# Performance work log

Measured on AMD Instinct MI355X. Metric: run time of the kernel, lower is better.

Reference implementation:

```python
import jax, jax.numpy as jnp
import numpy as np

B, S, D = 2, 2048, 2048
NH, NKV = 16, 4
HD = D // NH          # 128
Q_DIM = NH * HD       # 2048
KV_DIM = NKV * HD     # 512
N_REP = NH // NKV     # 4


def setup_inputs() -> dict:
    key = jax.random.key(0)
    k1, k2, k3, k4 = jax.random.split(key, 4)
    x = jax.random.normal(k1, (B, S, D), dtype=jnp.float32)
    freqs_cis = jax.random.normal(k2, (S, HD), dtype=jnp.float32)
    Wqkv = jax.random.normal(k3, (Q_DIM + 2 * KV_DIM, D), dtype=jnp.float32) * (D ** -0.5)
    Wo = jax.random.normal(k4, (D, Q_DIM), dtype=jnp.float32) * (Q_DIM ** -0.5)
    return {"x": x, "freqs_cis": freqs_cis, "Wqkv": Wqkv, "Wo": Wo}


def _apply_rope(xq, xk, freqs_cis):
    # xq: [B,S,NH,HD], xk: [B,S,NKV,HD], freqs_cis: [S,HD] viewed as [S,1,HD//2,2]
    f = freqs_cis.reshape(S, 1, HD // 2, 2)
    f0, f1 = f[..., 0], f[..., 1]  # broadcast over batch & heads

    def rot(t):
        shp = t.shape
        tp = t.reshape(*shp[:-1], HD // 2, 2)
        t0, t1 = tp[..., 0], tp[..., 1]
        # row1 = <x, (f0,f1)>;  row0 = <x, (f1,-f0)>  (matches torch flip+negate)
        row1 = t0 * f0 + t1 * f1
        row0 = t0 * f1 - t1 * f0
        return jnp.stack([row0, row1], axis=-1).reshape(shp)

    return rot(xq), rot(xk)


def reference(x, freqs_cis, Wqkv, Wo):
    # Fused QKV projection (exact path: all RLA sketch dims = 0)
    xqkv = jnp.einsum('bsd,od->bso', x, Wqkv)
    xq = xqkv[..., :Q_DIM].reshape(B, S, NH, HD)
    xk = xqkv[..., Q_DIM:Q_DIM + KV_DIM].reshape(B, S, NKV, HD)
    xv = xqkv[..., Q_DIM + KV_DIM:].reshape(B, S, NKV, HD)

    xq, xk = _apply_rope(xq, xk, freqs_cis)

    # [B,H,S,HD]
    xq = xq.transpose(0, 2, 1, 3)
    xk = xk.transpose(0, 2, 1, 3)
    xv = xv.transpose(0, 2, 1, 3)

    # GQA: repeat kv heads n_rep times
    xk = jnp.repeat(xk, N_REP, axis=1)
    xv = jnp.repeat(xv, N_REP, axis=1)

    scale = 1.0 / jnp.sqrt(jnp.asarray(HD, dtype=xq.dtype))
    scores = jnp.einsum('bhqd,bhkd->bhqk', xq, xk) * scale
    causal = jnp.tril(jnp.ones((S, S), dtype=bool))
    scores = jnp.where(causal, scores, jnp.finfo(scores.dtype).min)
    probs = jax.nn.softmax(scores, axis=-1)
    out = jnp.einsum('bhqk,bhkd->bhqd', probs, xv)  # [B,H,S,HD]

    out = out.transpose(0, 2, 1, 3).reshape(B, S, Q_DIM)
    return jnp.einsum('bsq,dq->bsd', out, Wo)
```

## Files before the change

### kernel.cpp

```cpp
#include <hip/hip_runtime.h>
#include <hip/hip_bf16.h>
#include <cstdint>
#include <cstddef>

#define B_ 2
#define S_ 2048
#define NH_ 16
#define NKV_ 4
#define HD_ 128
#define QDIM_ 2048
#define KVDIM_ 512
#define QKV_ 3072

typedef __attribute__((ext_vector_type(8))) short short8;
typedef __attribute__((ext_vector_type(4))) float float4v;

__device__ __forceinline__ float bf2f(short u) {
  union { unsigned int i; float f; } v;
  v.i = ((unsigned int)(unsigned short)u) << 16;
  return v.f;
}
__device__ __forceinline__ short f2bf(float f) {
  union { float f; unsigned int i; } v; v.f = f;
  unsigned int x = v.i;
  x += 0x7fffu + ((x >> 16) & 1u);
  return (short)(x >> 16);
}

__device__ __forceinline__ void async_copy16(void* lds, const void* g) {
  __builtin_amdgcn_global_load_lds(
      (const __attribute__((address_space(1))) void*)g,
      (__attribute__((address_space(3))) void*)lds, 16, 0, 0);
}

__global__ void f32_to_bf16(const float* __restrict__ src, short* __restrict__ dst,
                            int n8) {
  int id = blockIdx.x * 256 + threadIdx.x;
  if (id >= n8) return;
  const float* f = src + (size_t)id * 8;
  float4v a = *(const float4v*)(f);
  float4v b = *(const float4v*)(f + 4);
  short8 r;
#pragma unroll
  for (int e = 0; e < 4; ++e) { r[e] = f2bf(a[e]); r[4 + e] = f2bf(b[e]); }
  *(short8*)(dst + (size_t)id * 8) = r;
}

template <int N, int K, bool CF32>
__global__ __launch_bounds__(256)
void gemm_nt_bf16(const short* __restrict__ A, const short* __restrict__ Bm,
                  void* __restrict__ Cp) {
  __shared__ __align__(16) short sA[128 * 32];
  __shared__ __align__(16) short sB[128 * 32];
  const int tid = threadIdx.x;
  const int m0 = blockIdx.y * 128, n0 = blockIdx.x * 128;
  const int wave = tid >> 6, lane = tid & 63;
  const int wm = (wave & 1) << 6, wn = (wave >> 1) << 6;
  const int lm = lane & 15, kg = lane >> 4;

  float4v acc[4][4];
#pragma unroll
  for (int i = 0; i < 4; ++i)
#pragma unroll
    for (int j = 0; j < 4; ++j)
      acc[i][j] = (float4v){0.f, 0.f, 0.f, 0.f};

  const int r0 = tid >> 2, c0 = tid & 3;
  const short* gA0 = A + (size_t)(m0 + r0) * K + c0 * 8;
  const short* gA1 = gA0 + (size_t)64 * K;
  const short* gB0 = Bm + (size_t)(n0 + r0) * K + c0 * 8;
  const short* gB1 = gB0 + (size_t)64 * K;
  short* lA0 = sA + tid * 8;
  short* lA1 = sA + 2048 + tid * 8;
  short* lB0 = sB + tid * 8;
  short* lB1 = sB + 2048 + tid * 8;

  for (int k0 = 0; k0 < K; k0 += 32) {
    async_copy16(lA0, gA0 + k0);
    async_copy16(lA1, gA1 + k0);
    async_copy16(lB0, gB0 + k0);
    async_copy16(lB1, gB1 + k0);
    __syncthreads();

    short8 a[4], b[4];
#pragma unroll
    for (int i = 0; i < 4; ++i)
      a[i] = *(const short8*)(sA + (wm + i * 16 + lm) * 32 + kg * 8);
#pragma unroll
    for (int j = 0; j < 4; ++j)
      b[j] = *(const short8*)(sB + (wn + j * 16 + lm) * 32 + kg * 8);
#pragma unroll
    for (int i = 0; i < 4; ++i)
#pragma unroll
      for (int j = 0; j < 4; ++j)
        acc[i][j] = __builtin_amdgcn_mfma_f32_16x16x32_bf16(a[i], b[j], acc[i][j], 0, 0, 0);
    __syncthreads();
  }

#pragma unroll
  for (int i = 0; i < 4; ++i) {
    const int rb = m0 + wm + i * 16 + kg * 4;
#pragma unroll
    for (int j = 0; j < 4; ++j) {
      const int cc = n0 + wn + j * 16 + lm;
#pragma unroll
      for (int r = 0; r < 4; ++r) {
        if constexpr (CF32)
          ((float*)Cp)[(size_t)(rb + r) * N + cc] = acc[i][j][r];
        else
          ((short*)Cp)[(size_t)(rb + r) * N + cc] = f2bf(acc[i][j][r]);
      }
    }
  }
}

__global__ void rope_split(const short* __restrict__ xqkv, const float* __restrict__ freqs,
                           short* __restrict__ Qr, short* __restrict__ Kr,
                           short* __restrict__ Vv) {
  const int id = blockIdx.x * 256 + threadIdx.x;
  const int i = id / (QKV_ / 8);
  const int c8 = id % (QKV_ / 8);
  const int col = c8 * 8;
  const int b = i >> 11, s = i & (S_ - 1);
  short8 xv = *(const short8*)(xqkv + (size_t)i * QKV_ + col);
  if (col < QDIM_ + KVDIM_) {
    int d;
    short* dst;
    if (col < QDIM_) {
      int hh = col >> 7; d = col & 127;
      dst = Qr + ((size_t)(b * NH_ + hh) * S_ + s) * HD_ + d;
    } else {
      int cc = col - QDIM_;
      int hh = cc >> 7; d = cc & 127;
      dst = Kr + ((size_t)(b * NKV_ + hh) * S_ + s) * HD_ + d;
    }
    const float* fp = freqs + (size_t)s * HD_ + d;
    float4v fa = *(const float4v*)(fp);
    float4v fb = *(const float4v*)(fp + 4);
    float ff[8] = {fa[0], fa[1], fa[2], fa[3], fb[0], fb[1], fb[2], fb[3]};
    short8 ov;
#pragma unroll
    for (int pp = 0; pp < 4; ++pp) {
      float t0 = bf2f(xv[2 * pp]), t1 = bf2f(xv[2 * pp + 1]);
      float f0 = ff[2 * pp], f1 = ff[2 * pp + 1];
      ov[2 * pp]     = f2bf(t0 * f1 - t1 * f0);
      ov[2 * pp + 1] = f2bf(t0 * f0 + t1 * f1);
    }
    *(short8*)dst = ov;
  } else {
    int cc = col - QDIM_ - KVDIM_;
    int hh = cc >> 7, d = cc & 127;
    *(short8*)(Vv + ((size_t)(b * NKV_ + hh) * S_ + s) * HD_ + d) = xv;
  }
}

#define TK 64
#define KP 136
#define VP 72

__global__ __launch_bounds__(256)
void attn_causal(const short* __restrict__ Q, const short* __restrict__ K,
                 const short* __restrict__ V, short* __restrict__ O) {
  const int pair = blockIdx.x;
  const int bh = blockIdx.y;
  const int b = bh >> 4, h = bh & 15;
  const int kvh = h >> 2;
  const int tid = threadIdx.x, wave = tid >> 6, lane = tid & 63;
  const int lm = lane & 15, kg = lane >> 4;

  __shared__ __align__(16) short sK[TK * KP];
  __shared__ __align__(16) short sVt[HD_ * VP];
  __shared__ __align__(16) short sP[64 * VP];

  const short* Qb = Q + (size_t)(b * NH_ + h) * S_ * HD_;
  const short* Kb = K + (size_t)(b * NKV_ + kvh) * S_ * HD_;
  const short* Vb = V + (size_t)(b * NKV_ + kvh) * S_ * HD_;

  const int vd = tid & 127, vg = tid >> 7;

  for (int half = 0; half < 2; ++half) {
    const int qt = (half == 0) ? pair : 31 - pair;
    const int q0w = qt * 64 + wave * 16;

    short8 qf[4];
#pragma unroll
    for (int kk = 0; kk < 4; ++kk)
      qf[kk] = *(const short8*)(Qb + (size_t)(q0w + lm) * HD_ + kk * 32 + kg * 8);

    float mrow[4], lrow[4];
    float4v o[8];
#pragma unroll
    for (int r = 0; r < 4; ++r) { mrow[r] = -1e9f; lrow[r] = 0.f; }
#pragma unroll
    for (int df = 0; df < 8; ++df) o[df] = (float4v){0.f, 0.f, 0.f, 0.f};

    const int ntiles = qt + 1;
    for (int j = 0; j < ntiles; ++j) {
      const int k0 = j * TK;
      short8 kv[4];
#pragma unroll
      for (int c = 0; c < 4; ++c) {
        int ch = tid + 256 * c;
        int row = ch >> 4, kc = ch & 15;
        kv[c] = *(const short8*)(Kb + (size_t)(k0 + row) * HD_ + kc * 8);
      }
      unsigned short vvv[4][8];
#pragma unroll
      for (int c = 0; c < 4; ++c) {
        int kc = vg * 4 + c;
#pragma unroll
        for (int jj = 0; jj < 8; ++jj)
          vvv[c][jj] = (unsigned short)Vb[(size_t)(k0 + kc * 8 + jj) * HD_ + vd];
      }
      __syncthreads();
#pragma unroll
      for (int c = 0; c < 4; ++c) {
        int ch = tid + 256 * c;
        int row = ch >> 4, kc = ch & 15;
        *(short8*)(sK + row * KP + kc * 8) = kv[c];
      }
#pragma unroll
      for (int c = 0; c < 4; ++c) {
        int kc = vg * 4 + c;
        short8 w;
#pragma unroll
        for (int jj = 0; jj < 8; ++jj) w[jj] = (short)vvv[c][jj];
        *(short8*)(sVt + vd * VP + kc * 8) = w;
      }
      __syncthreads();

      float4v sf[4];
#pragma unroll
      for (int nj = 0; nj < 4; ++nj) sf[nj] = (float4v){0.f, 0.f, 0.f, 0.f};
#pragma unroll
      for (int kk = 0; kk < 4; ++kk) {
        int kd = kk * 4 + kg;
#pragma unroll
        for (int nj = 0; nj < 4; ++nj) {
          short8 bf = *(const short8*)(sK + (nj * 16 + lm) * KP + kd * 8);
          sf[nj] = __builtin_amdgcn_mfma_f32_16x16x32_bf16(qf[kk], bf, sf[nj], 0, 0, 0);
        }
      }

      const float scale = 0.08838834764831845f;
      const bool diag = (j == qt);
#pragma unroll
      for (int r = 0; r < 4; ++r) {
        float pv[4];
        float mx = -3e38f;
        if (diag) {
          const int qloc = wave * 16 + kg * 4 + r;
#pragma unroll
          for (int nj = 0; nj < 4; ++nj) {
            float v = ((nj * 16 + lm) <= qloc) ? sf[nj][r] * scale : -3e38f;
            pv[nj] = v; mx = fmaxf(mx, v);
          }
        } else {
#pragma unroll
          for (int nj = 0; nj < 4; ++nj) {
            float v = sf[nj][r] * scale;
            pv[nj] = v; mx = fmaxf(mx, v);
          }
        }
        mx = fmaxf(mx, __shfl_xor(mx, 1, 64));
        mx = fmaxf(mx, __shfl_xor(mx, 2, 64));
        mx = fmaxf(mx, __shfl_xor(mx, 4, 64));
        mx = fmaxf(mx, __shfl_xor(mx, 8, 64));
        float mold = mrow[r];
        float mnew = fmaxf(mold, mx);
        float alpha = __expf(fminf(mold - mnew, 0.f));
        float rs = 0.f;
#pragma unroll
        for (int nj = 0; nj < 4; ++nj) {
          float e = __expf(fminf(pv[nj] - mnew, 0.f));
          rs += e;
          sP[(wave * 16 + kg * 4 + r) * VP + nj * 16 + lm] = f2bf(e);
        }
        rs += __shfl_xor(rs, 1, 64);
        rs += __shfl_xor(rs, 2, 64);
        rs += __shfl_xor(rs, 4, 64);
        rs += __shfl_xor(rs, 8, 64);
        mrow[r] = mnew;
        lrow[r] = lrow[r] * alpha + rs;
#pragma unroll
        for (int df = 0; df < 8; ++df) o[df][r] *= alpha;
      }

#pragma unroll
      for (int kst = 0; kst < 2; ++kst) {
        short8 pa = *(const short8*)(sP + (wave * 16 + lm) * VP + kst * 32 + kg * 8);
#pragma unroll
        for (int df = 0; df < 8; ++df) {
          short8 vf = *(const short8*)(sVt + (df * 16 + lm) * VP + kst * 32 + kg * 8);
          o[df] = __builtin_amdgcn_mfma_f32_16x16x32_bf16(pa, vf, o[df], 0, 0, 0);
        }
      }
    }

#pragma unroll
    for (int r = 0; r < 4; ++r) {
      float inv = 1.f / lrow[r];
      const size_t rowoff =
          (size_t)(b * S_ + q0w + kg * 4 + r) * QDIM_ + h * HD_;
#pragma unroll
      for (int df = 0; df < 8; ++df)
        O[rowoff + df * 16 + lm] = f2bf(o[df][r] * inv);
    }
  }
}

extern "C" void kernel_launch(void* const* d_in, const int* in_sizes, int n_in,
                              void* d_out, int out_size, void* d_ws, size_t ws_size,
                              hipStream_t stream) {
  const float* x     = (const float*)d_in[0];
  const float* freqs = (const float*)d_in[1];
  const float* Wqkv  = (const float*)d_in[2];
  const float* Wo    = (const float*)d_in[3];
  float* out = (float*)d_out;

  short* ws     = (short*)d_ws;
  short* xb     = ws;
  short* Wob    = ws;
  short* Wqkvb  = ws + (size_t)4096 * 2048;
  short* xqkv   = Wqkvb + (size_t)QKV_ * 2048;
  short* attn   = xqkv;
  short* Qr     = xqkv + (size_t)4096 * QKV_;
  short* Kr     = Qr + (size_t)B_ * NH_ * S_ * HD_;
  short* Vv     = Kr + (size_t)B_ * NKV_ * S_ * HD_;

  f32_to_bf16<<<(4096 * 2048 / 8) / 256, 256, 0, stream>>>(x, xb, 4096 * 2048 / 8);
  f32_to_bf16<<<(QKV_ * 2048 / 8) / 256, 256, 0, stream>>>(Wqkv, Wqkvb, QKV_ * 2048 / 8);
  gemm_nt_bf16<QKV_, 2048, false>
      <<<dim3(QKV_ / 128, 4096 / 128), 256, 0, stream>>>(xb, Wqkvb, xqkv);
  f32_to_bf16<<<(2048 * 2048 / 8) / 256, 256, 0, stream>>>(Wo, Wob, 2048 * 2048 / 8);
  rope_split<<<(B_ * S_ * QKV_ / 8) / 256, 256, 0, stream>>>(xqkv, freqs, Qr, Kr, Vv);
  attn_causal<<<dim3(16, B_ * NH_), 256, 0, stream>>>(Qr, Kr, Vv, attn);
  gemm_nt_bf16<2048, 2048, true>
      <<<dim3(2048 / 128, 4096 / 128), 256, 0, stream>>>(attn, Wob, out);
}
```

Baseline: 350.3 us.

## Pre-transpose V globally and load K/V tiles via async swizzled LDS copies

Adds a transpose_v kernel that writes V as [d][s], so attention can load V^T tiles with 16-byte asynchronous global-to-LDS copies instead of scalar strided gathers and a register transpose. K and V tiles now use an XOR swizzle in place of padded LDS rows, and the softmax scale is folded into Q during RoPE. The cost is an extra kernel launch and an extra pass over V, plus a trailing barrier per tile. The code relies on an async_copy16 helper, presumably defined in the part not shown, and keeps a leftover no-op loop.

```diff
diff --git a/kernel.cpp b/kernel.cpp
--- a/kernel.cpp
+++ b/kernel.cpp
@@ -126,13 +126,16 @@
   if (col < QDIM_ + KVDIM_) {
     int d;
     short* dst;
+    float sc;
     if (col < QDIM_) {
       int hh = col >> 7; d = col & 127;
       dst = Qr + ((size_t)(b * NH_ + hh) * S_ + s) * HD_ + d;
+      sc = 0.08838834764831845f;
     } else {
       int cc = col - QDIM_;
       int hh = cc >> 7; d = cc & 127;
       dst = Kr + ((size_t)(b * NKV_ + hh) * S_ + s) * HD_ + d;
+      sc = 1.0f;
     }
     const float* fp = freqs + (size_t)s * HD_ + d;
     float4v fa = *(const float4v*)(fp);
@@ -143,8 +146,8 @@
     for (int pp = 0; pp < 4; ++pp) {
       float t0 = bf2f(xv[2 * pp]), t1 = bf2f(xv[2 * pp + 1]);
       float f0 = ff[2 * pp], f1 = ff[2 * pp + 1];
-      ov[2 * pp]     = f2bf(t0 * f1 - t1 * f0);
-      ov[2 * pp + 1] = f2bf(t0 * f0 + t1 * f1);
+      ov[2 * pp]     = f2bf((t0 * f1 - t1 * f0) * sc);
+      ov[2 * pp + 1] = f2bf((t0 * f0 + t1 * f1) * sc);
     }
     *(short8*)dst = ov;
   } else {
@@ -154,13 +157,37 @@
   }
 }
 
+__global__ void transpose_v(const short* __restrict__ Vv, short* __restrict__ Vt) {
+  __shared__ short t[64][72];
+  const int s0 = blockIdx.x * 64, d0 = blockIdx.y * 64;
+  const short* src = Vv + (size_t)blockIdx.z * S_ * HD_;
+  short* dst = Vt + (size_t)blockIdx.z * S_ * HD_;
+  const int tid = threadIdx.x;
+#pragma unroll
+  for (int c = 0; c < 2; ++c) {
+    int ch = tid + 256 * c;
+    int row = ch >> 3, kc = ch & 7;
+    *(short8*)(&t[row][kc * 8]) =
+        *(const short8*)(src + (size_t)(s0 + row) * HD_ + d0 + kc * 8);
+  }
+  __syncthreads();
+#pragma unroll
+  for (int c = 0; c < 2; ++c) {
+    int ch = tid + 256 * c;
+    int drow = ch >> 3, sc = ch & 7;
+    short8 w;
+#pragma unroll
+    for (int j = 0; j < 8; ++j) w[j] = t[sc * 8 + j][drow];
+    *(short8*)(dst + (size_t)(d0 + drow) * S_ + s0 + sc * 8) = w;
+  }
+}
+
 #define TK 64
-#define KP 136
 #define VP 72
 
 __global__ __launch_bounds__(256)
 void attn_causal(const short* __restrict__ Q, const short* __restrict__ K,
-                 const short* __restrict__ V, short* __restrict__ O) {
+                 const short* __restrict__ Vt, short* __restrict__ O) {
   const int pair = blockIdx.x;
   const int bh = blockIdx.y;
   const int b = bh >> 4, h = bh & 15;
@@ -168,15 +195,16 @@
   const int tid = threadIdx.x, wave = tid >> 6, lane = tid & 63;
   const int lm = lane & 15, kg = lane >> 4;
 
-  __shared__ __align__(16) short sK[TK * KP];
-  __shared__ __align__(16) short sVt[HD_ * VP];
+  __shared__ __align__(16) short sK[TK * HD_];
+  __shared__ __align__(16) short sVt[HD_ * TK];
   __shared__ __align__(16) short sP[64 * VP];
 
   const short* Qb = Q + (size_t)(b * NH_ + h) * S_ * HD_;
   const short* Kb = K + (size_t)(b * NKV_ + kvh) * S_ * HD_;
-  const short* Vb = V + (size_t)(b * NKV_ + kvh) * S_ * HD_;
-
-  const int vd = tid & 127, vg = tid >> 7;
+  const short* Vtb = Vt + (size_t)(b * NKV_ + kvh) * S_ * HD_;
+
+  const int krow0 = tid >> 4, kkc0 = tid & 15;
+  const int vrow0 = tid >> 3, vkc0 = tid & 7;
 
   for (int half = 0; half < 2; ++half) {
     const int qt = (half == 0) ? pair : 31 - pair;
@@ -197,35 +225,25 @@
     const int ntiles = qt + 1;
     for (int j = 0; j < ntiles; ++j) {
       const int k0 = j * TK;
-      short8 kv[4];
+#pragma unroll
+      for (int c = 0; c < 4; ++c) {
+        int ch = tid + 256 * c;
+        int row = (c & 1) ? (krow0 + 16 * (c >> 0)) : krow0;
+        (void)row;
+      }
 #pragma unroll
       for (int c = 0; c < 4; ++c) {
         int ch = tid + 256 * c;
         int row = ch >> 4, kc = ch & 15;
-        kv[c] = *(const short8*)(Kb + (size_t)(k0 + row) * HD_ + kc * 8);
-      }
-      unsigned short vvv[4][8];
-#pragma unroll
-      for (int c = 0; c < 4; ++c) {
-        int kc = vg * 4 + c;
-#pragma unroll
-        for (int jj = 0; jj < 8; ++jj)
-          vvv[c][jj] = (unsigned short)Vb[(size_t)(k0 + kc * 8 + jj) * HD_ + vd];
-      }
-      __syncthreads();
+        async_copy16(sK + ch * 8,
+                     Kb + (size_t)(k0 + row) * HD_ + (kc ^ (row & 7)) * 8);
+      }
 #pragma unroll
       for (int c = 0; c < 4; ++c) {
         int ch = tid + 256 * c;
-        int row = ch >> 4, kc = ch & 15;
-        *(short8*)(sK + row * KP + kc * 8) = kv[c];
-      }
-#pragma unroll
-      for (int c = 0; c < 4; ++c) {
-        int kc = vg * 4 + c;
-        short8 w;
-#pragma unroll
-        for (int jj = 0; jj < 8; ++jj) w[jj] = (short)vvv[c][jj];
-        *(short8*)(sVt + vd * VP + kc * 8) = w;
+        int row = ch >> 3, kc = ch & 7;
+        async_copy16(sVt + ch * 8,
+                     Vtb + (size_t)row * S_ + k0 + (kc ^ (row & 7)) * 8);
       }
       __syncthreads();
 
@@ -237,12 +255,12 @@
         int kd = kk * 4 + kg;
 #pragma unroll
         for (int nj = 0; nj < 4; ++nj) {
-          short8 bf = *(const short8*)(sK + (nj * 16 + lm) * KP + kd * 8);
+          int n = nj * 16 + lm;
+          short8 bf = *(const short8*)(sK + n * HD_ + (kd ^ (n & 7)) * 8);
           sf[nj] = __builtin_amdgcn_mfma_f32_16x16x32_bf16(qf[kk], bf, sf[nj], 0, 0, 0);
         }
       }
 
-      const float scale = 0.08838834764831845f;
       const bool diag = (j == qt);
 #pragma unroll
       for (int r = 0; r < 4; ++r) {
@@ -252,13 +270,13 @@
           const int qloc = wave * 16 + kg * 4 + r;
 #pragma unroll
           for (int nj = 0; nj < 4; ++nj) {
-            float v = ((nj * 16 + lm) <= qloc) ? sf[nj][r] * scale : -3e38f;
+            float v = ((nj * 16 + lm) <= qloc) ? sf[nj][r] : -3e38f;
             pv[nj] = v; mx = fmaxf(mx, v);
           }
         } else {
 #pragma unroll
           for (int nj = 0; nj < 4; ++nj) {
-            float v = sf[nj][r] * scale;
+            float v = sf[nj][r];
             pv[nj] = v; mx = fmaxf(mx, v);
           }
         }
@@ -289,12 +307,15 @@
 #pragma unroll
       for (int kst = 0; kst < 2; ++kst) {
         short8 pa = *(const short8*)(sP + (wave * 16 + lm) * VP + kst * 32 + kg * 8);
+        int kd = kst * 4 + kg;
 #pragma unroll
         for (int df = 0; df < 8; ++df) {
-          short8 vf = *(const short8*)(sVt + (df * 16 + lm) * VP + kst * 32 + kg * 8);
+          int n = df * 16 + lm;
+          short8 vf = *(const short8*)(sVt + n * TK + (kd ^ (n & 7)) * 8);
           o[df] = __builtin_amdgcn_mfma_f32_16x16x32_bf16(pa, vf, o[df], 0, 0, 0);
         }
       }
+      __syncthreads();
     }
 
 #pragma unroll
@@ -327,6 +348,7 @@
   short* Qr     = xqkv + (size_t)4096 * QKV_;
   short* Kr     = Qr + (size_t)B_ * NH_ * S_ * HD_;
   short* Vv     = Kr + (size_t)B_ * NKV_ * S_ * HD_;
+  short* Vtg    = Vv + (size_t)B_ * NKV_ * S_ * HD_;
 
   f32_to_bf16<<<(4096 * 2048 / 8) / 256, 256, 0, stream>>>(x, xb, 4096 * 2048 / 8);
   f32_to_bf16<<<(QKV_ * 2048 / 8) / 256, 256, 0, stream>>>(Wqkv, Wqkvb, QKV_ * 2048 / 8);
@@ -334,7 +356,8 @@
       <<<dim3(QKV_ / 128, 4096 / 128), 256, 0, stream>>>(xb, Wqkvb, xqkv);
   f32_to_bf16<<<(2048 * 2048 / 8) / 256, 256, 0, stream>>>(Wo, Wob, 2048 * 2048 / 8);
   rope_split<<<(B_ * S_ * QKV_ / 8) / 256, 256, 0, stream>>>(xqkv, freqs, Qr, Kr, Vv);
-  attn_causal<<<dim3(16, B_ * NH_), 256, 0, stream>>>(Qr, Kr, Vv, attn);
+  transpose_v<<<dim3(S_ / 64, HD_ / 64, B_ * NKV_), 256, 0, stream>>>(Vv, Vtg);
+  attn_causal<<<dim3(16, B_ * NH_), 256, 0, stream>>>(Qr, Kr, Vtg, attn);
   gemm_nt_bf16<2048, 2048, true>
       <<<dim3(2048 / 128, 4096 / 128), 256, 0, stream>>>(attn, Wob, out);
 }
```

Measured after the change: 337.6 us. -3.6%, faster.
